# Optimization experiments

Hardware: AMD Instinct MI355X
Metric: run time of the kernel (lower is better)

The kernel has to match this reference:

```python
import jax, jax.numpy as jnp
import numpy as np

B, S, D, E, TOP_K = 16, 2048, 240, 8, 2


def setup_inputs() -> dict:
    key = jax.random.key(0)
    k1, k2, k3 = jax.random.split(key, 3)
    scale = 1.0 / np.sqrt(D)
    return {
        "x": jax.random.normal(k1, (B, S, D), dtype=jnp.float32),
        "gate_w": jax.random.normal(k2, (E, D), dtype=jnp.float32) * scale,
        "gate_b": jnp.zeros((E,), dtype=jnp.float32),
        "expert_w": jax.random.normal(k3, (E, D, D), dtype=jnp.float32) * scale,
        "expert_b": jnp.zeros((E, D), dtype=jnp.float32),
    }


def reference(x, gate_w, gate_b, expert_w, expert_b):
    # Gating: softmax over experts, pick top-k, renormalize.
    logits = jnp.einsum("bsd,ed->bse", x, gate_w) + gate_b          # [B,S,E]
    gate_weights = jax.nn.softmax(logits, axis=-1)
    topk_w, topk_i = jax.lax.top_k(gate_weights, TOP_K)             # [B,S,K]
    topk_w = topk_w / jnp.sum(topk_w, axis=-1, keepdims=True)
    # Scatter renormalized top-k weights back to dense per-expert weights.
    onehot = jax.nn.one_hot(topk_i, E, dtype=x.dtype)               # [B,S,K,E]
    w_full = jnp.sum(topk_w[..., None] * onehot, axis=-2)           # [B,S,E]
    # Expert linears (torch Linear: y = x @ W^T + b), combined by gate weight.
    h = jnp.einsum("bsd,eod->bseo", x, expert_w) + expert_b         # [B,S,E,D]
    return jnp.einsum("bseo,bse->bso", h, w_full)                   # [B,S,D]
```

## Files before the change

kernel.cpp:

```cpp
#include <hip/hip_runtime.h>
#include <hip/hip_bf16.h>

#define TOKENS 32768
#define Dm 240
#define DP 256
#define NE 8
#define BK 32
#define NCHUNK 8
#define TILE_M 64
#define NB 64

typedef __bf16 bf16x8 __attribute__((ext_vector_type(8)));
typedef float  f32x4  __attribute__((ext_vector_type(4)));

__device__ __forceinline__ float b2f(unsigned short u) {
    union { unsigned int i; float f; } v; v.i = ((unsigned int)u) << 16; return v.f;
}
__device__ __forceinline__ float b2f_lo(unsigned u) {
    union { unsigned int i; float f; } v; v.i = u << 16; return v.f;
}
__device__ __forceinline__ float b2f_hi(unsigned u) {
    union { unsigned int i; float f; } v; v.i = u & 0xFFFF0000u; return v.f;
}
__device__ __forceinline__ unsigned short f2b(float f) {
    unsigned int i = __builtin_bit_cast(unsigned int, f);
    unsigned int r = (i + 0x7FFFu + ((i >> 16) & 1u)) >> 16;
    return (unsigned short)r;
}
__device__ __forceinline__ unsigned short f2h(float f) {
    _Float16 h = (_Float16)f;
    union { _Float16 h; unsigned short u; } v; v.h = h; return v.u;
}
__device__ __forceinline__ float h2f(unsigned short u) {
    union { _Float16 h; unsigned short u; } v; v.u = u; return (float)v.h;
}
__device__ __forceinline__ uint4 pack8(float4 a, float4 b) {
    union { unsigned short u[8]; uint4 v; } r;
    r.u[0] = f2b(a.x); r.u[1] = f2b(a.y); r.u[2] = f2b(a.z); r.u[3] = f2b(a.w);
    r.u[4] = f2b(b.x); r.u[5] = f2b(b.y); r.u[6] = f2b(b.z); r.u[7] = f2b(b.w);
    return r.v;
}

__device__ __forceinline__ void gload_lds16(const void* g, void* l) {
    __builtin_amdgcn_global_load_lds(
        (const __attribute__((address_space(1))) void*)g,
        (__attribute__((address_space(3))) void*)l,
        16, 0, 0);
}

__global__ void detect_kernel(const unsigned short* __restrict__ x, int* flag,
                              int* __restrict__ cnt) {
    int lane = threadIdx.x;
    cnt[lane] = 0;
    int hits = 0;
    for (int i = lane; i < 2048; i += 64) {
        unsigned e = (x[i] >> 7) & 0xFFu;
        if (e >= 0xC0u) hits++;
    }
    #pragma unroll
    for (int off = 32; off >= 1; off >>= 1) hits += __shfl_xor(hits, off, 64);
    if (lane == 0) flag[0] = (hits > 8) ? 1 : 0;
}

__global__ __launch_bounds__(256) void wconv_kernel(
    const void* __restrict__ ewv, const void* __restrict__ ebv,
    const int* __restrict__ flag,
    unsigned short* __restrict__ wpad, float* __restrict__ ebpad)
{
    const bool f32 = (*flag != 0);
    int gidx = blockIdx.x * 256 + threadIdx.x;

    if (gidx < NE * DP) {
        int e = gidx >> 8, n = gidx & 255;
        float bv = 0.f;
        if (n < Dm)
            bv = f32 ? ((const float*)ebv)[e * Dm + n]
                     : b2f(((const unsigned short*)ebv)[e * Dm + n]);
        ebpad[gidx] = bv;
    }

    int n = gidx & 255;
    int s = (gidx >> 8) & 3;
    int c = (gidx >> 10) & 7;
    int e = gidx >> 13;
    int k = c * 32 + s * 8;
    uint4 v = make_uint4(0, 0, 0, 0);
    if (n < Dm && k < Dm) {
        if (f32) {
            const float* src = (const float*)ewv + ((long)e * Dm + n) * Dm + k;
            v = pack8(*(const float4*)src, *(const float4*)(src + 4));
        } else {
            v = *(const uint4*)((const unsigned short*)ewv + ((long)e * Dm + n) * Dm + k);
        }
    }
    *(uint4*)&wpad[(long)gidx * 8] = v;
}

__global__ __launch_bounds__(128) void gate_kernel(
    const void* __restrict__ xv, const void* __restrict__ gwv,
    const void* __restrict__ gbv, const int* __restrict__ flag,
    int* __restrict__ cnt, unsigned* __restrict__ rt,
    unsigned short* __restrict__ xpad)
{
    const bool f32 = (*flag != 0);
    __shared__ float gws[NE * Dm];
    __shared__ int h[NB];
    __shared__ int base[NB];

    int tid = threadIdx.x;
    if (tid < NB) h[tid] = 0;
    for (int i = tid; i < NE * Dm; i += 128)
        gws[i] = f32 ? ((const float*)gwv)[i]
                     : b2f(((const unsigned short*)gwv)[i]);
    __syncthreads();

    int t = blockIdx.x * 128 + tid;
    float acc[NE];
    #pragma unroll
    for (int e = 0; e < NE; e++)
        acc[e] = f32 ? ((const float*)gbv)[e]
                     : b2f(((const unsigned short*)gbv)[e]);

    unsigned short* xo = xpad + (long)t * DP;
    if (f32) {
        const float* xf = (const float*)xv + (long)t * Dm;
        for (int k = 0; k < Dm; k += 8) {
            float4 xa = *(const float4*)&xf[k];
            float4 xb = *(const float4*)&xf[k + 4];
            *(uint4*)&xo[k] = pack8(xa, xb);
            #pragma unroll
            for (int e = 0; e < NE; e++) {
                float4 ga = *(const float4*)&gws[e * Dm + k];
                float4 gb4 = *(const float4*)&gws[e * Dm + k + 4];
                acc[e] += xa.x * ga.x + xa.y * ga.y + xa.z * ga.z + xa.w * ga.w
                        + xb.x * gb4.x + xb.y * gb4.y + xb.z * gb4.z + xb.w * gb4.w;
            }
        }
    } else {
        const unsigned short* xb = (const unsigned short*)xv + (long)t * Dm;
        for (int k = 0; k < Dm; k += 8) {
            uint4 xq = *(const uint4*)&xb[k];
            *(uint4*)&xo[k] = xq;
            float x0 = b2f_lo(xq.x), x1 = b2f_hi(xq.x);
            float x2 = b2f_lo(xq.y), x3 = b2f_hi(xq.y);
            float x4 = b2f_lo(xq.z), x5 = b2f_hi(xq.z);
            float x6 = b2f_lo(xq.w), x7 = b2f_hi(xq.w);
            #pragma unroll
            for (int e = 0; e < NE; e++) {
                float4 ga = *(const float4*)&gws[e * Dm + k];
                float4 gb4 = *(const float4*)&gws[e * Dm + k + 4];
                acc[e] += x0 * ga.x + x1 * ga.y + x2 * ga.z + x3 * ga.w
                        + x4 * gb4.x + x5 * gb4.y + x6 * gb4.z + x7 * gb4.w;
            }
        }
    }
    {
        uint4 z = make_uint4(0, 0, 0, 0);
        *(uint4*)&xo[Dm] = z;
        *(uint4*)&xo[Dm + 8] = z;
    }

    float l0 = -1e30f; int e0 = 0;
    #pragma unroll
    for (int e = 0; e < NE; e++) if (acc[e] > l0) { l0 = acc[e]; e0 = e; }
    float l1 = -1e30f; int e1 = 0;
    #pragma unroll
    for (int e = 0; e < NE; e++) if (e != e0 && acc[e] > l1) { l1 = acc[e]; e1 = e; }
    float w0 = 1.f / (1.f + __expf(l1 - l0));

    int b = e0 * 8 + e1;
    __syncthreads();
    atomicAdd(&h[b], 1);
    __syncthreads();
    if (tid < NB) {
        base[tid] = atomicAdd(&cnt[tid], h[tid]);
        h[tid] = 0;
    }
    __syncthreads();
    {
        int o = atomicAdd(&h[b], 1);
        rt[b * TOKENS + base[b] + o] = ((unsigned)t << 16) | (unsigned)f2h(w0);
    }
}

__global__ __launch_bounds__(256, 2) void expert_kernel(
    const unsigned short* __restrict__ xp,
    const unsigned short* __restrict__ wp,
    const float* __restrict__ ebpad,
    const int* __restrict__ flag,
    const int* __restrict__ cnt, const unsigned* __restrict__ rt,
    void* __restrict__ outv)
{
    __shared__ __align__(16) unsigned short Wc[2][2][4][256][8];
    __shared__ __align__(16) unsigned short Xc[2][4][64][8];
    __shared__ int cntS[NB];

    int tid = threadIdx.x;
    if (tid < NB) cntS[tid] = cnt[tid];
    __syncthreads();

    int fid = blockIdx.x;
    int b = -1, t = 0, accn = 0;
    for (int i = 0; i < NB; i++) {
        int ti = (cntS[i] + 63) >> 6;
        if (fid < accn + ti) { b = i; t = fid - accn; break; }
        accn += ti;
    }
    if (b < 0) return;
    int e0 = b >> 3, e1 = b & 7;
    int ne = cntS[b];
    int m0 = t * TILE_M;
    int rows = min(TILE_M, ne - m0);

    int lane = tid & 63;
    int wv   = tid >> 6;

    unsigned rvp = rt[b * TOKENS + min(m0 + lane, ne - 1)];
    int   tokL = (int)(rvp >> 16);
    float w0L  = h2f((unsigned short)(rvp & 0xFFFFu));

    const unsigned short* xsrc = xp + (long)tokL * DP + wv * 8;
    const unsigned short* wb0  = wp + (long)e0 * NCHUNK * 8192;
    const unsigned short* wb1  = wp + (long)e1 * NCHUNK * 8192;
    unsigned short* WcF = &Wc[0][0][0][0][0];
    const int bufW = 2 * 8192;

    auto stage = [&](int c, int buf) {
        gload_lds16(xsrc + c * BK, &Xc[buf][wv][0][0]);
        #pragma unroll
        for (int i = 0; i < 4; i++) {
            int u = wv * 4 + i;
            gload_lds16(wb0 + (long)c * 8192 + u * 512 + lane * 8,
                        WcF + buf * bufW + u * 512);
            gload_lds16(wb1 + (long)c * 8192 + u * 512 + lane * 8,
                        WcF + buf * bufW + 8192 + u * 512);
        }
    };

    stage(0, 0);
    __syncthreads();

    int frow = lane & 15;
    int slot = lane >> 4;
    f32x4 acc0[4][4] = {};
    f32x4 acc1[4][4] = {};

    for (int c = 0; c < NCHUNK; c++) {
        int buf = c & 1;
        if (c + 1 < NCHUNK) stage(c + 1, buf ^ 1);
        bf16x8 a[4];
        #pragma unroll
        for (int mt = 0; mt < 4; mt++)
            a[mt] = *(const bf16x8*)&Xc[buf][slot][mt * 16 + frow][0];
        #pragma unroll
        for (int nt = 0; nt < 4; nt++) {
            bf16x8 b0v = *(const bf16x8*)&Wc[buf][0][slot][wv * 64 + nt * 16 + frow][0];
            bf16x8 b1v = *(const bf16x8*)&Wc[buf][1][slot][wv * 64 + nt * 16 + frow][0];
            #pragma unroll
            for (int mt = 0; mt < 4; mt++) {
                acc0[mt][nt] = __builtin_amdgcn_mfma_f32_16x16x32_bf16(
                    a[mt], b0v, acc0[mt][nt], 0, 0, 0);
                acc1[mt][nt] = __builtin_amdgcn_mfma_f32_16x16x32_bf16(
                    a[mt], b1v, acc1[mt][nt], 0, 0, 0);
            }
        }
        __syncthreads();
    }

    const bool f32o = (*flag != 0);
    int colg = lane & 15;
    int rq   = (lane >> 4) << 2;
    float b0n[4], b1n[4];
    #pragma unroll
    for (int nt = 0; nt < 4; nt++) {
        int n = wv * 64 + nt * 16 + colg;
        b0n[nt] = ebpad[e0 * DP + n];
        b1n[nt] = ebpad[e1 * DP + n];
    }
    #pragma unroll
    for (int mt = 0; mt < 4; mt++) {
        #pragma unroll
        for (int r = 0; r < 4; r++) {
            int m = mt * 16 + rq + r;
            int   tok = __shfl(tokL, m);
            float w0  = __shfl(w0L, m);
            float w1  = 1.f - w0;
            if (m < rows) {
                #pragma unroll
                for (int nt = 0; nt < 4; nt++) {
                    int n = wv * 64 + nt * 16 + colg;
                    if (n < Dm) {
                        float val = (acc0[mt][nt][r] + b0n[nt]) * w0
                                  + (acc1[mt][nt][r] + b1n[nt]) * w1;
                        long idx = (long)tok * Dm + n;
                        if (f32o) ((float*)outv)[idx] = val;
                        else      ((unsigned short*)outv)[idx] = f2b(val);
                    }
                }
            }
        }
    }
}

__global__ void init_kernel(int* cnt) {
    if (threadIdx.x < 16) cnt[threadIdx.x] = 0;
}

__global__ void zero_kernel(void* outv, const int* flag, int nelem) {
    long i = (long)blockIdx.x * blockDim.x + threadIdx.x;
    long stride = (long)gridDim.x * blockDim.x;
    if (*flag) {
        float* o = (float*)outv;
        for (; i < nelem; i += stride) o[i] = 0.f;
    } else {
        unsigned* o = (unsigned*)outv;
        long n = nelem >> 1;
        for (; i < n; i += stride) o[i] = 0u;
    }
}

template<bool FP32>
__global__ __launch_bounds__(256) void gate_fb_kernel(
    const void* __restrict__ xv, const void* __restrict__ gwv,
    const void* __restrict__ gbv, const int* __restrict__ flag,
    int* __restrict__ cnt, unsigned* __restrict__ rt, int cap)
{
    if ((*flag != 0) != FP32) return;
    __shared__ unsigned rv[256];
    __shared__ int h[16];
    __shared__ int base[16];

    int tid = threadIdx.x;
    if (tid < 16) h[tid] = 0;
    int t = blockIdx.x * 256 + tid;

    float acc[NE];
    #pragma unroll
    for (int e = 0; e < NE; e++)
        acc[e] = FP32 ? ((const float*)gbv)[e]
                      : b2f(((const unsigned short*)gbv)[e]);

    if (FP32) {
        const float* xf  = (const float*)xv + (long)t * Dm;
        const float* gwf = (const float*)gwv;
        for (int k = 0; k < Dm; k += 8) {
            float4 xa = *(const float4*)&xf[k];
            float4 xb = *(const float4*)&xf[k + 4];
            #pragma unroll
            for (int e = 0; e < NE; e++) {
                float4 ga = *(const float4*)&gwf[e * Dm + k];
                float4 gb = *(const float4*)&gwf[e * Dm + k + 4];
                acc[e] += xa.x * ga.x + xa.y * ga.y + xa.z * ga.z + xa.w * ga.w
                        + xb.x * gb.x + xb.y * gb.y + xb.z * gb.z + xb.w * gb.w;
            }
        }
    } else {
        const unsigned short* xb  = (const unsigned short*)xv + (long)t * Dm;
        const unsigned short* gwb = (const unsigned short*)gwv;
        for (int k = 0; k < Dm; k += 8) {
            uint4 xq = *(const uint4*)&xb[k];
            float x0 = b2f_lo(xq.x), x1 = b2f_hi(xq.x);
            float x2 = b2f_lo(xq.y), x3 = b2f_hi(xq.y);
            float x4 = b2f_lo(xq.z), x5 = b2f_hi(xq.z);
            float x6 = b2f_lo(xq.w), x7 = b2f_hi(xq.w);
            #pragma unroll
            for (int e = 0; e < NE; e++) {
                uint4 gq = *(const uint4*)&gwb[e * Dm + k];
                acc[e] += x0 * b2f_lo(gq.x) + x1 * b2f_hi(gq.x)
                        + x2 * b2f_lo(gq.y) + x3 * b2f_hi(gq.y)
                        + x4 * b2f_lo(gq.z) + x5 * b2f_hi(gq.z)
                        + x6 * b2f_lo(gq.w) + x7 * b2f_hi(gq.w);
            }
        }
    }

    float l0 = -1e30f; int e0 = 0;
    #pragma unroll
    for (int e = 0; e < NE; e++) if (acc[e] > l0) { l0 = acc[e]; e0 = e; }
    float l1 = -1e30f; int e1 = 0;
    #pragma unroll
    for (int e = 0; e < NE; e++) if (e != e0 && acc[e] > l1) { l1 = acc[e]; e1 = e; }
    float w0 = 1.f / (1.f + __expf(l1 - l0));

    rv[tid] = ((unsigned)e1 << 20) | ((unsigned)e0 << 16) | (unsigned)f2h(w0);
    __syncthreads();

    {
        unsigned v = rv[tid];
        atomicAdd(&h[(v >> 16) & 7], 1);
        atomicAdd(&h[8 + ((v >> 20) & 7)], 1);
    }
    __syncthreads();

    if (tid < 16) {
        base[tid] = atomicAdd(&cnt[tid], h[tid]);
        h[tid] = 0;
    }
    __syncthreads();

    {
        unsigned v = rv[tid];
        int tt = blockIdx.x * 256 + tid;
        int a0 = (v >> 16) & 7;
        int a1 = (v >> 20) & 7;
        unsigned short hw0 = (unsigned short)(v & 0xFFFFu);
        int o0 = atomicAdd(&h[a0], 1);
        int p0 = base[a0] + o0;
        if (p0 < cap) rt[a0 * cap + p0] = ((unsigned)tt << 16) | hw0;
        int o1 = atomicAdd(&h[8 + a1], 1);
        int p1 = base[8 + a1] + o1;
        if (p1 < cap) rt[(8 + a1) * cap + p1] = ((unsigned)tt << 16) | (unsigned)f2h(1.f - h2f(hw0));
    }
}

template<bool FP32>
__global__ __launch_bounds__(256) void expert_fb_kernel(
    const void* __restrict__ xv, const void* __restrict__ ewv,
    const void* __restrict__ ebv, const int* __restrict__ flag,
    const int* __restrict__ cnt, const unsigned* __restrict__ rt, int cap,
    void* __restrict__ outv, int slotBase, int accumulate)
{
    if ((*flag != 0) != FP32) return;
    int e = blockIdx.y;
    int tile = blockIdx.x;
    int bucket = slotBase + e;
    int ne = min(cnt[bucket], cap);
    int m0 = tile * TILE_M;
    if (m0 >= ne) return;
    int rows = min(TILE_M, ne - m0);

    __shared__ __align__(16) unsigned short Wcf[2][256][40];
    __shared__ __align__(16) unsigned short Xcf[2][TILE_M][40];
    __shared__ int   tokS[TILE_M];
    __shared__ float twS[TILE_M];

    int tid = threadIdx.x;
    if (tid < TILE_M) {
        int i = min(m0 + tid, ne - 1);
        unsigned v = rt[bucket * cap + i];
        tokS[tid] = (int)(v >> 16);
        twS[tid]  = (tid < rows) ? h2f((unsigned short)(v & 0xFFFFu)) : 0.f;
    }
    __syncthreads();

    int srow = tid >> 2;
    int part = tid & 3;

    auto stage = [&](int c, int buf) {
        int kk = c * BK + part * 8;
        bool kvalid = (kk < Dm);
        if (FP32) {
            const float* xf = (const float*)xv;
            const float* Wf = (const float*)ewv + e * Dm * Dm;
            uint4 xq = make_uint4(0, 0, 0, 0);
            if (kvalid) {
                const float* s = &xf[(long)tokS[srow] * Dm + kk];
                xq = pack8(*(const float4*)s, *(const float4*)(s + 4));
            }
            *(uint4*)&Xcf[buf][srow][part * 8] = xq;
            #pragma unroll
            for (int it = 0; it < 4; it++) {
                int n = srow + it * 64;
                uint4 wq = make_uint4(0, 0, 0, 0);
                if (kvalid && n < Dm) {
                    const float* s = &Wf[(long)n * Dm + kk];
                    wq = pack8(*(const float4*)s, *(const float4*)(s + 4));
                }
                *(uint4*)&Wcf[buf][n][part * 8] = wq;
            }
        } else {
            const unsigned short* xb = (const unsigned short*)xv;
            const unsigned short* Wb = (const unsigned short*)ewv + e * Dm * Dm;
            uint4 xq = make_uint4(0, 0, 0, 0);
            if (kvalid) xq = *(const uint4*)&xb[(long)tokS[srow] * Dm + kk];
            *(uint4*)&Xcf[buf][srow][part * 8] = xq;
            #pragma unroll
            for (int it = 0; it < 4; it++) {
                int n = srow + it * 64;
                uint4 wq = make_uint4(0, 0, 0, 0);
                if (kvalid && n < Dm) wq = *(const uint4*)&Wb[(long)n * Dm + kk];
                *(uint4*)&Wcf[buf][n][part * 8] = wq;
            }
        }
    };

    int lane = tid & 63;
    int wv   = tid >> 6;
    int frow = lane & 15;
    int koff = (lane >> 4) * 8;

    f32x4 acc[TILE_M / 16][4] = {};

    stage(0, 0);
    __syncthreads();
    for (int c = 0; c < NCHUNK; c++) {
        int buf = c & 1;
        bf16x8 a[TILE_M / 16], b[4];
        #pragma unroll
        for (int mt = 0; mt < TILE_M / 16; mt++)
            a[mt] = *(const bf16x8*)&Xcf[buf][mt * 16 + frow][koff];
        #pragma unroll
        for (int nt = 0; nt < 4; nt++)
            b[nt] = *(const bf16x8*)&Wcf[buf][wv * 64 + nt * 16 + frow][koff];
        if (c + 1 < NCHUNK) stage(c + 1, (c + 1) & 1);
        #pragma unroll
        for (int mt = 0; mt < TILE_M / 16; mt++)
            #pragma unroll
            for (int nt = 0; nt < 4; nt++)
                acc[mt][nt] = __builtin_amdgcn_mfma_f32_16x16x32_bf16(
                    a[mt], b[nt], acc[mt][nt], 0, 0, 0);
        __syncthreads();
    }

    int colg  = lane & 15;
    int rquad = (lane >> 4) * 4;
    #pragma unroll
    for (int nt = 0; nt < 4; nt++) {
        int n = wv * 64 + nt * 16 + colg;
        if (n >= Dm) continue;
        float bnv = FP32 ? ((const float*)ebv)[e * Dm + n]
                         : b2f(((const unsigned short*)ebv)[e * Dm + n]);
        #pragma unroll
        for (int mt = 0; mt < TILE_M / 16; mt++) {
            #pragma unroll
            for (int r = 0; r < 4; r++) {
                int m = mt * 16 + rquad + r;
                if (m < rows) {
                    float val = (acc[mt][nt][r] + bnv) * twS[m];
                    long idx = (long)tokS[m] * Dm + n;
                    if (FP32) {
                        float* o = (float*)outv + idx;
                        *o = accumulate ? (*o + val) : val;
                    } else {
                        unsigned short* o = (unsigned short*)outv + idx;
                        *o = accumulate ? f2b(b2f(*o) + val) : f2b(val);
                    }
                }
            }
        }
    }
}

extern "C" void kernel_launch(void* const* d_in, const int* in_sizes, int n_in,
                              void* d_out, int out_size, void* d_ws, size_t ws_size,
                              hipStream_t stream) {
    const void* x  = d_in[0];
    const void* gw = d_in[1];
    const void* gb = d_in[2];
    const void* ew = d_in[3];
    const void* eb = d_in[4];

    char* ws = (char*)d_ws;
    int* flag = (int*)ws;
    int* cnt  = (int*)(ws + 64);

    const size_t EB_OFF = 320;
    const size_t RT_OFF = EB_OFF + (size_t)NE * DP * 4;
    const size_t XP_OFF = RT_OFF + (size_t)NB * TOKENS * 4;
    const size_t WP_OFF = XP_OFF + (size_t)TOKENS * DP * 2;
    const size_t NEEDED = WP_OFF + (size_t)NE * NCHUNK * 8192 * 2;

    if (ws_size >= NEEDED) {
        float*          ebpad = (float*)(ws + EB_OFF);
        unsigned*       rt    = (unsigned*)(ws + RT_OFF);
        unsigned short* xpad  = (unsigned short*)(ws + XP_OFF);
        unsigned short* wpad  = (unsigned short*)(ws + WP_OFF);

        detect_kernel<<<1, 64, 0, stream>>>((const unsigned short*)x, flag, cnt);
        wconv_kernel<<<256, 256, 0, stream>>>(ew, eb, flag, wpad, ebpad);
        gate_kernel<<<TOKENS / 128, 128, 0, stream>>>(x, gw, gb, flag, cnt, rt, xpad);
        expert_kernel<<<TOKENS / TILE_M + NB, 256, 0, stream>>>(
            xpad, wpad, ebpad, flag, cnt, rt, d_out);
    } else {
        unsigned* rt = (unsigned*)(ws + 128);
        long capl = ((long)ws_size - 128) / (16 * sizeof(unsigned));
        if (capl > TOKENS) capl = TOKENS;
        if (capl < 64) capl = 64;
        int cap = (int)capl;
        int tiles = (cap + TILE_M - 1) / TILE_M;
        bool lossless = (cap >= TOKENS);
        int acc0 = lossless ? 0 : 1;

        detect_kernel<<<1, 64, 0, stream>>>((const unsigned short*)x, flag, cnt);
        init_kernel<<<1, 64, 0, stream>>>(cnt);
        gate_fb_kernel<false><<<TOKENS / 256, 256, 0, stream>>>(x, gw, gb, flag, cnt, rt, cap);
        gate_fb_kernel<true ><<<TOKENS / 256, 256, 0, stream>>>(x, gw, gb, flag, cnt, rt, cap);
        if (!lossless)
            zero_kernel<<<1024, 256, 0, stream>>>(d_out, flag, out_size);
        expert_fb_kernel<false><<<dim3(tiles, NE), 256, 0, stream>>>(x, ew, eb, flag, cnt, rt, cap, d_out, 0, acc0);
        expert_fb_kernel<true ><<<dim3(tiles, NE), 256, 0, stream>>>(x, ew, eb, flag, cnt, rt, cap, d_out, 0, acc0);
        expert_fb_kernel<false><<<dim3(tiles, NE), 256, 0, stream>>>(x, ew, eb, flag, cnt, rt, cap, d_out, 8, 1);
        expert_fb_kernel<true ><<<dim3(tiles, NE), 256, 0, stream>>>(x, ew, eb, flag, cnt, rt, cap, d_out, 8, 1);
    }
}
```

Measured before the change: 160.2 us.

## Fuse dtype detection into kernels, parallelize gating per token, stream weights directly

Removes the separate detect kernel: each wconv and gate block detects the input dtype redundantly, and wconv zeroes the counters. The gate kernel now spreads each token across 8 threads with shuffle reductions and keeps bf16 gate weights in LDS. The expert kernel stages all X chunks into LDS at once and reads expert weights directly from global memory into registers, dropping the double-buffered weight LDS pipeline and its per-chunk barriers. It also remaps block IDs across 8 groups. Risks include higher global load latency on weights without LDS staging, and a race because wconv zeroes cnt while the gate kernel relies only on stream ordering.

```diff
diff --git a/kernel.cpp b/kernel.cpp
--- a/kernel.cpp
+++ b/kernel.cpp
@@ -48,27 +48,38 @@
         16, 0, 0);
 }
 
-__global__ void detect_kernel(const unsigned short* __restrict__ x, int* flag,
-                              int* __restrict__ cnt) {
-    int lane = threadIdx.x;
-    cnt[lane] = 0;
+__device__ __forceinline__ bool block_detect_f32(const unsigned short* x,
+                                                 int tid, int* dh) {
+    if (tid == 0) *dh = 0;
+    __syncthreads();
+    uint4 q = *(const uint4*)&x[tid * 8];
+    unsigned w[4] = {q.x, q.y, q.z, q.w};
     int hits = 0;
-    for (int i = lane; i < 2048; i += 64) {
-        unsigned e = (x[i] >> 7) & 0xFFu;
-        if (e >= 0xC0u) hits++;
-    }
-    #pragma unroll
-    for (int off = 32; off >= 1; off >>= 1) hits += __shfl_xor(hits, off, 64);
-    if (lane == 0) flag[0] = (hits > 8) ? 1 : 0;
+    #pragma unroll
+    for (int i = 0; i < 4; i++) {
+        if ((((w[i] & 0xFFFFu) >> 7) & 0xFFu) >= 0xC0u) hits++;
+        if ((((w[i] >> 16)      >> 7) & 0xFFu) >= 0xC0u) hits++;
+    }
+    if (hits) atomicAdd(dh, hits);
+    __syncthreads();
+    return *dh > 8;
 }
 
 __global__ __launch_bounds__(256) void wconv_kernel(
     const void* __restrict__ ewv, const void* __restrict__ ebv,
-    const int* __restrict__ flag,
+    const unsigned short* __restrict__ xus,
+    int* __restrict__ flag, int* __restrict__ cnt,
     unsigned short* __restrict__ wpad, float* __restrict__ ebpad)
 {
-    const bool f32 = (*flag != 0);
-    int gidx = blockIdx.x * 256 + threadIdx.x;
+    __shared__ int dh;
+    int tid = threadIdx.x;
+    const bool f32 = block_detect_f32(xus, tid, &dh);
+    if (blockIdx.x == 0) {
+        if (tid == 0) flag[0] = f32 ? 1 : 0;
+        if (tid < NB) cnt[tid] = 0;
+    }
+
+    int gidx = blockIdx.x * 256 + tid;
 
     if (gidx < NE * DP) {
         int e = gidx >> 8, n = gidx & 255;
@@ -96,90 +107,125 @@
     *(uint4*)&wpad[(long)gidx * 8] = v;
 }
 
-__global__ __launch_bounds__(128) void gate_kernel(
+__global__ __launch_bounds__(256) void gate_kernel(
     const void* __restrict__ xv, const void* __restrict__ gwv,
-    const void* __restrict__ gbv, const int* __restrict__ flag,
+    const void* __restrict__ gbv,
     int* __restrict__ cnt, unsigned* __restrict__ rt,
     unsigned short* __restrict__ xpad)
 {
-    const bool f32 = (*flag != 0);
-    __shared__ float gws[NE * Dm];
+    __shared__ float gwsF[NE * Dm];
     __shared__ int h[NB];
     __shared__ int base[NB];
+    __shared__ int dh;
 
     int tid = threadIdx.x;
     if (tid < NB) h[tid] = 0;
-    for (int i = tid; i < NE * Dm; i += 128)
-        gws[i] = f32 ? ((const float*)gwv)[i]
-                     : b2f(((const unsigned short*)gwv)[i]);
-    __syncthreads();
-
-    int t = blockIdx.x * 128 + tid;
-    float acc[NE];
-    #pragma unroll
-    for (int e = 0; e < NE; e++)
-        acc[e] = f32 ? ((const float*)gbv)[e]
-                     : b2f(((const unsigned short*)gbv)[e]);
-
+    const bool f32 = block_detect_f32((const unsigned short*)xv, tid, &dh);
+
+    if (f32) {
+        if (tid < 240) {
+            const float* s = (const float*)gwv + tid * 8;
+            float4 a = *(const float4*)s;
+            float4 b4 = *(const float4*)(s + 4);
+            float* d = &gwsF[tid * 8];
+            *(float4*)d = a; *(float4*)(d + 4) = b4;
+        }
+    } else {
+        if (tid < 240) {
+            unsigned short* gb16 = (unsigned short*)gwsF;
+            *(uint4*)&gb16[tid * 8] =
+                *(const uint4*)((const unsigned short*)gwv + tid * 8);
+        }
+    }
+    __syncthreads();
+
+    int grp = tid >> 3;
+    int j   = tid & 7;
+    int t   = blockIdx.x * 32 + grp;
+
+    float acc[NE] = {0.f, 0.f, 0.f, 0.f, 0.f, 0.f, 0.f, 0.f};
     unsigned short* xo = xpad + (long)t * DP;
+
     if (f32) {
         const float* xf = (const float*)xv + (long)t * Dm;
-        for (int k = 0; k < Dm; k += 8) {
-            float4 xa = *(const float4*)&xf[k];
-            float4 xb = *(const float4*)&xf[k + 4];
-            *(uint4*)&xo[k] = pack8(xa, xb);
-            #pragma unroll
-            for (int e = 0; e < NE; e++) {
-                float4 ga = *(const float4*)&gws[e * Dm + k];
-                float4 gb4 = *(const float4*)&gws[e * Dm + k + 4];
-                acc[e] += xa.x * ga.x + xa.y * ga.y + xa.z * ga.z + xa.w * ga.w
-                        + xb.x * gb4.x + xb.y * gb4.y + xb.z * gb4.z + xb.w * gb4.w;
+        #pragma unroll
+        for (int i = 0; i < 4; i++) {
+            int g = j + 8 * i;
+            if (g < 30) {
+                float4 xa = *(const float4*)&xf[g * 8];
+                float4 xb = *(const float4*)&xf[g * 8 + 4];
+                *(uint4*)&xo[g * 8] = pack8(xa, xb);
+                #pragma unroll
+                for (int e = 0; e < NE; e++) {
+                    const float* gp = &gwsF[e * Dm + g * 8];
+                    float4 ga = *(const float4*)gp;
+                    float4 gc = *(const float4*)(gp + 4);
+                    acc[e] += xa.x * ga.x + xa.y * ga.y + xa.z * ga.z + xa.w * ga.w
+                            + xb.x * gc.x + xb.y * gc.y + xb.z * gc.z + xb.w * gc.w;
+                }
+            } else {
+                *(uint4*)&xo[g * 8] = make_uint4(0, 0, 0, 0);
             }
         }
     } else {
         const unsigned short* xb = (const unsigned short*)xv + (long)t * Dm;
-        for (int k = 0; k < Dm; k += 8) {
-            uint4 xq = *(const uint4*)&xb[k];
-            *(uint4*)&xo[k] = xq;
-            float x0 = b2f_lo(xq.x), x1 = b2f_hi(xq.x);
-            float x2 = b2f_lo(xq.y), x3 = b2f_hi(xq.y);
-            float x4 = b2f_lo(xq.z), x5 = b2f_hi(xq.z);
-            float x6 = b2f_lo(xq.w), x7 = b2f_hi(xq.w);
-            #pragma unroll
-            for (int e = 0; e < NE; e++) {
-                float4 ga = *(const float4*)&gws[e * Dm + k];
-                float4 gb4 = *(const float4*)&gws[e * Dm + k + 4];
-                acc[e] += x0 * ga.x + x1 * ga.y + x2 * ga.z + x3 * ga.w
-                        + x4 * gb4.x + x5 * gb4.y + x6 * gb4.z + x7 * gb4.w;
-            }
-        }
-    }
-    {
-        uint4 z = make_uint4(0, 0, 0, 0);
-        *(uint4*)&xo[Dm] = z;
-        *(uint4*)&xo[Dm + 8] = z;
-    }
-
-    float l0 = -1e30f; int e0 = 0;
-    #pragma unroll
-    for (int e = 0; e < NE; e++) if (acc[e] > l0) { l0 = acc[e]; e0 = e; }
-    float l1 = -1e30f; int e1 = 0;
-    #pragma unroll
-    for (int e = 0; e < NE; e++) if (e != e0 && acc[e] > l1) { l1 = acc[e]; e1 = e; }
-    float w0 = 1.f / (1.f + __expf(l1 - l0));
-
-    int b = e0 * 8 + e1;
-    __syncthreads();
-    atomicAdd(&h[b], 1);
+        const unsigned short* gb16 = (const unsigned short*)gwsF;
+        #pragma unroll
+        for (int i = 0; i < 4; i++) {
+            int g = j + 8 * i;
+            if (g < 30) {
+                uint4 xq = *(const uint4*)&xb[g * 8];
+                *(uint4*)&xo[g * 8] = xq;
+                float x0 = b2f_lo(xq.x), x1 = b2f_hi(xq.x);
+                float x2 = b2f_lo(xq.y), x3 = b2f_hi(xq.y);
+                float x4 = b2f_lo(xq.z), x5 = b2f_hi(xq.z);
+                float x6 = b2f_lo(xq.w), x7 = b2f_hi(xq.w);
+                #pragma unroll
+                for (int e = 0; e < NE; e++) {
+                    uint4 gq = *(const uint4*)&gb16[e * Dm + g * 8];
+                    acc[e] += x0 * b2f_lo(gq.x) + x1 * b2f_hi(gq.x)
+                            + x2 * b2f_lo(gq.y) + x3 * b2f_hi(gq.y)
+                            + x4 * b2f_lo(gq.z) + x5 * b2f_hi(gq.z)
+                            + x6 * b2f_lo(gq.w) + x7 * b2f_hi(gq.w);
+                }
+            } else {
+                *(uint4*)&xo[g * 8] = make_uint4(0, 0, 0, 0);
+            }
+        }
+    }
+
+    #pragma unroll
+    for (int m = 1; m < 8; m <<= 1)
+        #pragma unroll
+        for (int e = 0; e < NE; e++)
+            acc[e] += __shfl_xor(acc[e], m, 64);
+
+    int bb = 0; float w0 = 0.f;
+    if (j == 0) {
+        #pragma unroll
+        for (int e = 0; e < NE; e++)
+            acc[e] += f32 ? ((const float*)gbv)[e]
+                          : b2f(((const unsigned short*)gbv)[e]);
+        float l0 = -1e30f; int e0 = 0;
+        #pragma unroll
+        for (int e = 0; e < NE; e++) if (acc[e] > l0) { l0 = acc[e]; e0 = e; }
+        float l1 = -1e30f; int e1 = 0;
+        #pragma unroll
+        for (int e = 0; e < NE; e++) if (e != e0 && acc[e] > l1) { l1 = acc[e]; e1 = e; }
+        w0 = 1.f / (1.f + __expf(l1 - l0));
+        bb = e0 * 8 + e1;
+        atomicAdd(&h[bb], 1);
+    }
     __syncthreads();
     if (tid < NB) {
-        base[tid] = atomicAdd(&cnt[tid], h[tid]);
+        int c = h[tid];
+        if (c) base[tid] = atomicAdd(&cnt[tid], c);
         h[tid] = 0;
     }
     __syncthreads();
-    {
-        int o = atomicAdd(&h[b], 1);
-        rt[b * TOKENS + base[b] + o] = ((unsigned)t << 16) | (unsigned)f2h(w0);
+    if (j == 0) {
+        int o = atomicAdd(&h[bb], 1);
+        rt[bb * TOKENS + base[bb] + o] = ((unsigned)t << 16) | (unsigned)f2h(w0);
     }
 }
 
@@ -191,15 +237,19 @@
     const int* __restrict__ cnt, const unsigned* __restrict__ rt,
     void* __restrict__ outv)
 {
-    __shared__ __align__(16) unsigned short Wc[2][2][4][256][8];
-    __shared__ __align__(16) unsigned short Xc[2][4][64][8];
+    __shared__ __align__(16) unsigned short Xc[NCHUNK][4][64][8];
     __shared__ int cntS[NB];
 
+    const bool f32o = (*flag != 0);
     int tid = threadIdx.x;
     if (tid < NB) cntS[tid] = cnt[tid];
     __syncthreads();
 
+    int nwg = gridDim.x;
     int fid = blockIdx.x;
+    if ((nwg & 7) == 0)
+        fid = (blockIdx.x & 7) * (nwg >> 3) + (blockIdx.x >> 3);
+
     int b = -1, t = 0, accn = 0;
     for (int i = 0; i < NB; i++) {
         int ti = (cntS[i] + 63) >> 6;
@@ -220,54 +270,43 @@
     float w0L  = h2f((unsigned short)(rvp & 0xFFFFu));
 
     const unsigned short* xsrc = xp + (long)tokL * DP + wv * 8;
-    const unsigned short* wb0  = wp + (long)e0 * NCHUNK * 8192;
-    const unsigned short* wb1  = wp + (long)e1 * NCHUNK * 8192;
-    unsigned short* WcF = &Wc[0][0][0][0][0];
-    const int bufW = 2 * 8192;
-
-    auto stage = [&](int c, int buf) {
-        gload_lds16(xsrc + c * BK, &Xc[buf][wv][0][0]);
-        #pragma unroll
-        for (int i = 0; i < 4; i++) {
-            int u = wv * 4 + i;
-            gload_lds16(wb0 + (long)c * 8192 + u * 512 + lane * 8,
-                        WcF + buf * bufW + u * 512);
-            gload_lds16(wb1 + (long)c * 8192 + u * 512 + lane * 8,
-                        WcF + buf * bufW + 8192 + u * 512);
-        }
-    };
-
-    stage(0, 0);
+    #pragma unroll
+    for (int c = 0; c < NCHUNK; c++)
+        gload_lds16(xsrc + c * BK, &Xc[c][wv][0][0]);
     __syncthreads();
 
     int frow = lane & 15;
     int slot = lane >> 4;
+    const unsigned short* wb0 = wp + (long)e0 * 65536 + slot * 2048
+                                   + (wv * 64 + frow) * 8;
+    const unsigned short* wb1 = wp + (long)e1 * 65536 + slot * 2048
+                                   + (wv * 64 + frow) * 8;
+
     f32x4 acc0[4][4] = {};
     f32x4 acc1[4][4] = {};
 
+    #pragma unroll
     for (int c = 0; c < NCHUNK; c++) {
-        int buf = c & 1;
-        if (c + 1 < NCHUNK) stage(c + 1, buf ^ 1);
-        bf16x8 a[4];
+        bf16x8 a[4], b0[4], b1[4];
         #pragma unroll
         for (int mt = 0; mt < 4; mt++)
-            a[mt] = *(const bf16x8*)&Xc[buf][slot][mt * 16 + frow][0];
+            a[mt] = *(const bf16x8*)&Xc[c][slot][mt * 16 + frow][0];
         #pragma unroll
         for (int nt = 0; nt < 4; nt++) {
-            bf16x8 b0v = *(const bf16x8*)&Wc[buf][0][slot][wv * 64 + nt * 16 + frow][0];
-            bf16x8 b1v = *(const bf16x8*)&Wc[buf][1][slot][wv * 64 + nt * 16 + frow][0];
+            b0[nt] = *(const bf16x8*)&wb0[c * 8192 + nt * 128];
+            b1[nt] = *(const bf16x8*)&wb1[c * 8192 + nt * 128];
+        }
+        #pragma unroll
+        for (int nt = 0; nt < 4; nt++)
             #pragma unroll
             for (int mt = 0; mt < 4; mt++) {
                 acc0[mt][nt] = __builtin_amdgcn_mfma_f32_16x16x32_bf16(
-                    a[mt], b0v, acc0[mt][nt], 0, 0, 0);
+                    a[mt], b0[nt], acc0[mt][nt], 0, 0, 0);
                 acc1[mt][nt] = __builtin_amdgcn_mfma_f32_16x16x32_bf16(
-                    a[mt], b1v, acc1[mt][nt], 0, 0, 0);
-            }
-        }
-        __syncthreads();
-    }
-
-    const bool f32o = (*flag != 0);
+                    a[mt], b1[nt], acc1[mt][nt], 0, 0, 0);
+            }
+    }
+
     int colg = lane & 15;
     int rq   = (lane >> 4) << 2;
     float b0n[4], b1n[4];
@@ -302,6 +341,20 @@
     }
 }
 
+__global__ void detect_kernel(const unsigned short* __restrict__ x, int* flag,
+                              int* __restrict__ cnt) {
+    int lane = threadIdx.x;
+    cnt[lane] = 0;
+    int hits = 0;
+    for (int i = lane; i < 2048; i += 64) {
+        unsigned e = (x[i] >> 7) & 0xFFu;
+        if (e >= 0xC0u) hits++;
+    }
+    #pragma unroll
+    for (int off = 32; off >= 1; off >>= 1) hits += __shfl_xor(hits, off, 64);
+    if (lane == 0) flag[0] = (hits > 8) ? 1 : 0;
+}
+
 __global__ void init_kernel(int* cnt) {
     if (threadIdx.x < 16) cnt[threadIdx.x] = 0;
 }
@@ -566,9 +619,9 @@
         unsigned short* xpad  = (unsigned short*)(ws + XP_OFF);
         unsigned short* wpad  = (unsigned short*)(ws + WP_OFF);
 
-        detect_kernel<<<1, 64, 0, stream>>>((const unsigned short*)x, flag, cnt);
-        wconv_kernel<<<256, 256, 0, stream>>>(ew, eb, flag, wpad, ebpad);
-        gate_kernel<<<TOKENS / 128, 128, 0, stream>>>(x, gw, gb, flag, cnt, rt, xpad);
+        wconv_kernel<<<256, 256, 0, stream>>>(ew, eb, (const unsigned short*)x,
+                                              flag, cnt, wpad, ebpad);
+        gate_kernel<<<TOKENS / 32, 256, 0, stream>>>(x, gw, gb, cnt, rt, xpad);
         expert_kernel<<<TOKENS / TILE_M + NB, 256, 0, stream>>>(
             xpad, wpad, ebpad, flag, cnt, rt, d_out);
     } else {
```

Result: faster. 145.7 us (-9.1%).
